# Performance work log

Hardware: AMD Instinct MI355X
Metric: run time of the kernel (lower is better)

## Reference

```python
import jax, jax.numpy as jnp
import numpy as np

N, T, D = 64, 1024, 64  # (batch*heads, seq_len==max_len, head_dim)
PADDING_NUM = -2.0**32 + 1.0


def setup_inputs() -> dict:
    key = jax.random.key(0)
    kq, kk, kv = jax.random.split(key, 3)
    q = jax.random.normal(kq, (N, T, D), dtype=jnp.float32)
    k = jax.random.normal(kk, (N, T, D), dtype=jnp.float32)
    v = jax.random.normal(kv, (N, T, D), dtype=jnp.float32)
    return {"q": q, "k": k, "v": v}


def reference(q, k, v):
    # attn = q @ k^T / sqrt(d_k)  -> (N, T_q, T_k)
    dk_norm = jnp.sqrt(jnp.asarray(k.shape[-1], dtype=jnp.float32))
    scores = jnp.einsum('bqd,bkd->bqk', q, k) / dk_norm
    # key padding mask: keys whose abs-sum is 0 are masked to padding_num
    key_mask = (jnp.sum(jnp.abs(k), axis=-1) != 0)[:, None, :]  # (N, 1, T_k)
    scores = jnp.where(key_mask, scores, PADDING_NUM)
    # causal (future) mask: cumsum of eye -> lower triangular keep-mask
    causal = jnp.tril(jnp.ones((T, T), dtype=bool))[None, :, :]  # (1, T, T)
    scores = jnp.where(causal, scores, PADDING_NUM)
    attn = jax.nn.softmax(scores, axis=-1)
    # dropout with training=False is identity
    return jnp.einsum('bqk,bkv->bqv', attn, v)
```

## Files before the change

### kernel.cpp

```cpp
#include <hip/hip_runtime.h>
#include <math.h>


#define N_HEADS 64
#define T_SEQ   1024
#define D_HEAD  64
#define QBLK    128
#define KVB     64
#define NQB     (T_SEQ / QBLK)
#define PADDING_NUM (-4294967295.0f)
#define KSTRIDE 144
#define VSTRIDE 144

typedef __attribute__((ext_vector_type(8)))  short bf16x8;
typedef __attribute__((ext_vector_type(16))) float f32x16;
typedef __attribute__((ext_vector_type(4)))  unsigned int uint4v;

union FragU { uint4v u; bf16x8 v; };

template<bool B> struct BoolC { static constexpr bool value = B; };

static __device__ __forceinline__ unsigned f2bf(float f) {
    union { float f; unsigned u; } c; c.f = f;
    return (c.u + 0x7fffu + ((c.u >> 16) & 1u)) >> 16;
}
static __device__ __forceinline__ unsigned pk2(float lo, float hi) {
    return f2bf(lo) | (f2bf(hi) << 16);
}
static __device__ __forceinline__ f32x16 zero16() {
    f32x16 z;
    #pragma unroll
    for (int i = 0; i < 16; ++i) z[i] = 0.f;
    return z;
}

__global__ __launch_bounds__(256)
void attn_fwd(const float* __restrict__ q, const float* __restrict__ k,
              const float* __restrict__ v, float* __restrict__ out) {
    __shared__ __align__(16) char  KT_lds[2][KVB * KSTRIDE];
    __shared__ __align__(16) char  VT_lds[2][D_HEAD * VSTRIDE];
    __shared__ __align__(16) float kadd[2][KVB];

    const int bx  = blockIdx.x;
    const int n   = bx & 63;
    const int qb  = (NQB - 1) - (bx >> 6);
    const int tid = threadIdx.x;
    const int w   = tid >> 6;
    const int l   = tid & 63;
    const int h   = l >> 5;
    const int ql  = l & 31;
    const int qrow = qb * QBLK + w * 32 + ql;

    const float* qg = q + (size_t)n * T_SEQ * D_HEAD;
    const float* kg = k + (size_t)n * T_SEQ * D_HEAD;
    const float* vg = v + (size_t)n * T_SEQ * D_HEAD;

    FragU qf[4];
    #pragma unroll
    for (int s = 0; s < 4; ++s) {
        const float* qp = qg + (size_t)qrow * D_HEAD + s * 16 + h * 8;
        float4 a = ((const float4*)qp)[0], b = ((const float4*)qp)[1];
        qf[s].u[0] = pk2(a.x * 0.125f, a.y * 0.125f);
        qf[s].u[1] = pk2(a.z * 0.125f, a.w * 0.125f);
        qf[s].u[2] = pk2(b.x * 0.125f, b.y * 0.125f);
        qf[s].u[3] = pk2(b.z * 0.125f, b.w * 0.125f);
    }

    f32x16 O0 = zero16(), O1 = zero16();
    float m = -INFINITY, l_sum = 0.f;

    float4 kbuf[2][2], vbuf[2][2];

    auto k_issue = [&](int t) {
        const float* base = kg + (size_t)t * KVB * D_HEAD;
        #pragma unroll
        for (int i = 0; i < 2; ++i) {
            int c = tid + 256 * i; int key = c >> 3, oct = c & 7;
            const float4* p = (const float4*)(base + key * D_HEAD + oct * 8);
            kbuf[i][0] = p[0]; kbuf[i][1] = p[1];
        }
    };
    auto v_issue = [&](int t) {
        const float* base = vg + (size_t)t * KVB * D_HEAD;
        #pragma unroll
        for (int i = 0; i < 2; ++i) {
            int c = tid + 256 * i; int kp = c & 31, dq = c >> 5;
            const float* p0 = base + (2 * kp) * D_HEAD + dq * 4;
            vbuf[i][0] = *(const float4*)p0;
            vbuf[i][1] = *(const float4*)(p0 + D_HEAD);
        }
    };
    auto kv_write = [&](int b) {
        #pragma unroll
        for (int i = 0; i < 2; ++i) {
            int c = tid + 256 * i; int key = c >> 3, oct = c & 7;
            float4 A = kbuf[i][0], B = kbuf[i][1];
            float s = fabsf(A.x) + fabsf(A.y) + fabsf(A.z) + fabsf(A.w)
                    + fabsf(B.x) + fabsf(B.y) + fabsf(B.z) + fabsf(B.w);
            s += __shfl_xor(s, 1); s += __shfl_xor(s, 2); s += __shfl_xor(s, 4);
            if (oct == 0) kadd[b][key] = (s != 0.f) ? 0.f : PADDING_NUM;
            uint4v w4;
            w4[0] = pk2(A.x, A.y); w4[1] = pk2(A.z, A.w);
            w4[2] = pk2(B.x, B.y); w4[3] = pk2(B.z, B.w);
            *(uint4v*)(KT_lds[b] + key * KSTRIDE + oct * 16) = w4;

            int kp = c & 31, dq = c >> 5;
            float4 VA = vbuf[i][0], VB = vbuf[i][1];
            *(unsigned*)(VT_lds[b] + (dq * 4 + 0) * VSTRIDE + kp * 4) = pk2(VA.x, VB.x);
            *(unsigned*)(VT_lds[b] + (dq * 4 + 1) * VSTRIDE + kp * 4) = pk2(VA.y, VB.y);
            *(unsigned*)(VT_lds[b] + (dq * 4 + 2) * VSTRIDE + kp * 4) = pk2(VA.z, VB.z);
            *(unsigned*)(VT_lds[b] + (dq * 4 + 3) * VSTRIDE + kp * 4) = pk2(VA.w, VB.w);
        }
    };

    auto process = [&](int b, int t, auto causal_c) {
        constexpr bool CAUSAL = decltype(causal_c)::value;
        const char* Kb = KT_lds[b];
        const char* Vb = VT_lds[b];

        f32x16 S[2];
        #pragma unroll
        for (int kgi = 0; kgi < 2; ++kgi) {
            f32x16 acc = zero16();
            #pragma unroll
            for (int s = 0; s < 4; ++s) {
                bf16x8 kf = *(const bf16x8*)(Kb + (kgi * 32 + ql) * KSTRIDE + s * 32 + h * 16);
                acc = __builtin_amdgcn_mfma_f32_32x32x16_bf16(kf, qf[s].v, acc, 0, 0, 0);
            }
            S[kgi] = acc;
        }

        float tmax = -INFINITY;
        #pragma unroll
        for (int kgi = 0; kgi < 2; ++kgi) {
            #pragma unroll
            for (int rq = 0; rq < 4; ++rq) {
                float4 kd = *(const float4*)&kadd[b][kgi * 32 + rq * 8 + 4 * h];
                #pragma unroll
                for (int j = 0; j < 4; ++j) {
                    int r = rq * 4 + j;
                    float sc = S[kgi][r] + ((const float*)&kd)[j];
                    if (CAUSAL) {
                        int key = t * KVB + kgi * 32 + rq * 8 + 4 * h + j;
                        sc = (key <= qrow) ? sc : PADDING_NUM;
                    }
                    S[kgi][r] = sc;
                    tmax = fmaxf(tmax, sc);
                }
            }
        }
        tmax = fmaxf(tmax, __shfl_xor(tmax, 32));

        const float newm = fmaxf(m, tmax);
        const float corr = __expf(m - newm);
        m = newm;
        l_sum *= corr;
        #pragma unroll
        for (int i = 0; i < 16; ++i) { O0[i] *= corr; O1[i] *= corr; }

        float ls = 0.f;
        #pragma unroll
        for (int kgi = 0; kgi < 2; ++kgi)
            #pragma unroll
            for (int r = 0; r < 16; ++r) {
                float p = __expf(S[kgi][r] - newm);
                S[kgi][r] = p;
                ls += p;
            }
        ls += __shfl_xor(ls, 32);
        l_sum += ls;

        #pragma unroll
        for (int kgi = 0; kgi < 2; ++kgi) {
            #pragma unroll
            for (int s2 = 0; s2 < 2; ++s2) {
                unsigned A0 = pk2(S[kgi][8 * s2 + 0], S[kgi][8 * s2 + 1]);
                unsigned A1 = pk2(S[kgi][8 * s2 + 2], S[kgi][8 * s2 + 3]);
                unsigned A2 = pk2(S[kgi][8 * s2 + 4], S[kgi][8 * s2 + 5]);
                unsigned A3 = pk2(S[kgi][8 * s2 + 6], S[kgi][8 * s2 + 7]);
                unsigned sw0 = (unsigned)__shfl_xor((int)A0, 32);
                unsigned sw1 = (unsigned)__shfl_xor((int)A1, 32);
                unsigned sw2 = (unsigned)__shfl_xor((int)A2, 32);
                unsigned sw3 = (unsigned)__shfl_xor((int)A3, 32);
                FragU pb;
                pb.u[0] = h ? sw2 : A0;
                pb.u[1] = h ? sw3 : A1;
                pb.u[2] = h ? A2 : sw0;
                pb.u[3] = h ? A3 : sw1;
                const int ksf = kgi * 2 + s2;
                bf16x8 vf0 = *(const bf16x8*)(Vb + (0 * 32 + ql) * VSTRIDE + ksf * 32 + h * 16);
                bf16x8 vf1 = *(const bf16x8*)(Vb + (1 * 32 + ql) * VSTRIDE + ksf * 32 + h * 16);
                O0 = __builtin_amdgcn_mfma_f32_32x32x16_bf16(vf0, pb.v, O0, 0, 0, 0);
                O1 = __builtin_amdgcn_mfma_f32_32x32x16_bf16(vf1, pb.v, O1, 0, 0, 0);
            }
        }
    };

    k_issue(0); v_issue(0);
    kv_write(0);
    __syncthreads();

    const int nt    = 2 * (qb + 1);
    const int tdiag = 2 * qb + (w >> 1);
    int buf = 0;
    for (int t = 0; t < nt; ++t) {
        if (t + 1 < nt) { k_issue(t + 1); v_issue(t + 1); }
        if (t < tdiag)       process(buf, t, BoolC<false>{});
        else if (t == tdiag) process(buf, t, BoolC<true>{});
        if (t + 1 < nt) kv_write(buf ^ 1);
        __syncthreads();
        buf ^= 1;
    }

    const float inv = 1.f / l_sum;
    #pragma unroll
    for (int g = 0; g < 2; ++g) {
        #pragma unroll
        for (int r = 0; r < 16; ++r) {
            int d = (r & 3) + 8 * (r >> 2) + 4 * h + 32 * g;
            float val = (g ? O1[r] : O0[r]) * inv;
            out[(size_t)n * T_SEQ * D_HEAD + (size_t)qrow * D_HEAD + d] = val;
        }
    }
}

extern "C" void kernel_launch(void* const* d_in, const int* in_sizes, int n_in,
                              void* d_out, int out_size, void* d_ws, size_t ws_size,
                              hipStream_t stream) {
    (void)d_ws; (void)ws_size; (void)in_sizes; (void)n_in; (void)out_size;
    const float* q = (const float*)d_in[0];
    const float* k = (const float*)d_in[1];
    const float* v = (const float*)d_in[2];
    float* o = (float*)d_out;
    dim3 grid(N_HEADS * NQB);
    dim3 block(256);
    hipLaunchKernelGGL(attn_fwd, grid, block, 0, stream, q, k, v, o);
}
```

Before: 49.15 us.

## Pair mirrored 64-row query blocks per workgroup for causal load balance, use exp2

```diff
diff --git a/kernel.cpp b/kernel.cpp
--- a/kernel.cpp
+++ b/kernel.cpp
@@ -1,16 +1,16 @@
 #include <hip/hip_runtime.h>
+#include <hip/hip_bf16.h>
 #include <math.h>
 
 
 #define N_HEADS 64
 #define T_SEQ   1024
 #define D_HEAD  64
-#define QBLK    128
 #define KVB     64
-#define NQB     (T_SEQ / QBLK)
 #define PADDING_NUM (-4294967295.0f)
 #define KSTRIDE 144
 #define VSTRIDE 144
+#define QSCALE  (0.125f * 1.4426950408889634f)
 
 typedef __attribute__((ext_vector_type(8)))  short bf16x8;
 typedef __attribute__((ext_vector_type(16))) float f32x16;
@@ -20,12 +20,10 @@
 
 template<bool B> struct BoolC { static constexpr bool value = B; };
 
-static __device__ __forceinline__ unsigned f2bf(float f) {
-    union { float f; unsigned u; } c; c.f = f;
-    return (c.u + 0x7fffu + ((c.u >> 16) & 1u)) >> 16;
-}
 static __device__ __forceinline__ unsigned pk2(float lo, float hi) {
-    return f2bf(lo) | (f2bf(hi) << 16);
+    union { __hip_bfloat162 h2; unsigned u; } c;
+    c.h2 = __float22bfloat162_rn(make_float2(lo, hi));
+    return c.u;
 }
 static __device__ __forceinline__ f32x16 zero16() {
     f32x16 z;
@@ -43,13 +41,15 @@
 
     const int bx  = blockIdx.x;
     const int n   = bx & 63;
-    const int qb  = (NQB - 1) - (bx >> 6);
+    const int pr  = bx >> 6;
     const int tid = threadIdx.x;
     const int w   = tid >> 6;
     const int l   = tid & 63;
     const int h   = l >> 5;
     const int ql  = l & 31;
-    const int qrow = qb * QBLK + w * 32 + ql;
+    const int sel  = (w ^ bx) & 1;
+    const int hs   = sel ? pr : (15 - pr);
+    const int qrow = hs * 64 + (w >> 1) * 32 + ql;
 
     const float* qg = q + (size_t)n * T_SEQ * D_HEAD;
     const float* kg = k + (size_t)n * T_SEQ * D_HEAD;
@@ -60,17 +60,16 @@
     for (int s = 0; s < 4; ++s) {
         const float* qp = qg + (size_t)qrow * D_HEAD + s * 16 + h * 8;
         float4 a = ((const float4*)qp)[0], b = ((const float4*)qp)[1];
-        qf[s].u[0] = pk2(a.x * 0.125f, a.y * 0.125f);
-        qf[s].u[1] = pk2(a.z * 0.125f, a.w * 0.125f);
-        qf[s].u[2] = pk2(b.x * 0.125f, b.y * 0.125f);
-        qf[s].u[3] = pk2(b.z * 0.125f, b.w * 0.125f);
+        qf[s].u[0] = pk2(a.x * QSCALE, a.y * QSCALE);
+        qf[s].u[1] = pk2(a.z * QSCALE, a.w * QSCALE);
+        qf[s].u[2] = pk2(b.x * QSCALE, b.y * QSCALE);
+        qf[s].u[3] = pk2(b.z * QSCALE, b.w * QSCALE);
     }
 
     f32x16 O0 = zero16(), O1 = zero16();
     float m = -INFINITY, l_sum = 0.f;
 
     float4 kbuf[2][2], vbuf[2][2];
-
     auto k_issue = [&](int t) {
         const float* base = kg + (size_t)t * KVB * D_HEAD;
         #pragma unroll
@@ -152,7 +151,7 @@
         tmax = fmaxf(tmax, __shfl_xor(tmax, 32));
 
         const float newm = fmaxf(m, tmax);
-        const float corr = __expf(m - newm);
+        const float corr = __builtin_amdgcn_exp2f(m - newm);
         m = newm;
         l_sum *= corr;
         #pragma unroll
@@ -163,7 +162,7 @@
         for (int kgi = 0; kgi < 2; ++kgi)
             #pragma unroll
             for (int r = 0; r < 16; ++r) {
-                float p = __expf(S[kgi][r] - newm);
+                float p = __builtin_amdgcn_exp2f(S[kgi][r] - newm);
                 S[kgi][r] = p;
                 ls += p;
             }
@@ -200,13 +199,12 @@
     kv_write(0);
     __syncthreads();
 
-    const int nt    = 2 * (qb + 1);
-    const int tdiag = 2 * qb + (w >> 1);
+    const int nt = 16 - pr;
     int buf = 0;
     for (int t = 0; t < nt; ++t) {
         if (t + 1 < nt) { k_issue(t + 1); v_issue(t + 1); }
-        if (t < tdiag)       process(buf, t, BoolC<false>{});
-        else if (t == tdiag) process(buf, t, BoolC<true>{});
+        if (t < hs)       process(buf, t, BoolC<false>{});
+        else if (t == hs) process(buf, t, BoolC<true>{});
         if (t + 1 < nt) kv_write(buf ^ 1);
         __syncthreads();
         buf ^= 1;
@@ -232,7 +230,7 @@
     const float* k = (const float*)d_in[1];
     const float* v = (const float*)d_in[2];
     float* o = (float*)d_out;
-    dim3 grid(N_HEADS * NQB);
+    dim3 grid(N_HEADS * 8);
     dim3 block(256);
     hipLaunchKernelGGL(attn_fwd, grid, block, 0, stream, q, k, v, o);
 }
```

After: 46.71 us. 5.0% less time.
